# Performance work log

Measured on AMD Instinct MI355X. Metric: run time of the kernel, lower is better.

Reference implementation:

```python
import jax, jax.numpy as jnp
import numpy as np

N = 100000   # nodes
E = 1600000  # edges
G = 100      # graphs
M = 32       # m_dim for all layers


def _lin(k, din, dout):
    return (jax.random.normal(k, (din, dout), jnp.float32) / np.sqrt(din)).astype(jnp.float32)


def setup_inputs() -> dict:
    key = jax.random.key(0)
    ks = jax.random.split(key, 32)
    inp = {}
    inp["x"] = jax.random.normal(ks[0], (N, 2), jnp.float32)
    inp["positions"] = jax.random.normal(ks[1], (N, 2), jnp.float32)
    inp["edge_index"] = jax.random.randint(ks[2], (2, E), 0, N)
    inp["edge_attr"] = jax.random.normal(ks[3], (E, 1), jnp.float32)
    inp["batch"] = jnp.sort(jax.random.randint(ks[4], (N,), 0, G))
    ki = 5
    dims = [(2, 32), (32, 32), (32, 32)]  # (feats_in, out_dim) per EGNN layer
    for l, (fi, fo) in enumerate(dims, 1):
        ein = 2 * fi + 1 + 1  # x_i, x_j, edge_attr(1), rel_dist(1)
        inp[f"e{l}W1"] = _lin(ks[ki], ein, 2 * ein); ki += 1
        inp[f"e{l}b1"] = jnp.zeros((2 * ein,), jnp.float32)
        inp[f"e{l}W2"] = _lin(ks[ki], 2 * ein, M); ki += 1
        inp[f"e{l}b2"] = jnp.zeros((M,), jnp.float32)
        inp[f"n{l}W1"] = _lin(ks[ki], fi + M, 2 * fo); ki += 1
        inp[f"n{l}b1"] = jnp.zeros((2 * fo,), jnp.float32)
        inp[f"n{l}W2"] = _lin(ks[ki], 2 * fo, fo); ki += 1
        inp[f"n{l}b2"] = jnp.zeros((fo,), jnp.float32)
    inp["linW"] = _lin(ks[ki], 32, 1)
    inp["linb"] = jnp.zeros((1,), jnp.float32)
    return inp


def _egnn_layer(xcat, ei, ea, eW1, eb1, eW2, eb2, nW1, nb1, nW2, nb2):
    # xcat: [N, 2 + f_in]; coors pass through (update_coors=False)
    coors, feats = xcat[:, :2], xcat[:, 2:]
    j, i = ei[0], ei[1]  # PyG convention: edge_index[0]=source j, [1]=target i
    rel = coors[j] - coors[i]                      # [E, 2]
    rel_dist = jnp.sum(rel * rel, -1, keepdims=True)  # [E, 1]
    e_in = jnp.concatenate([feats[i], feats[j], ea, rel_dist], -1)
    m_ij = jax.nn.silu(jax.nn.silu(e_in @ eW1 + eb1) @ eW2 + eb2)  # [E, M]
    m_i = jax.ops.segment_sum(m_ij, i, num_segments=xcat.shape[0])  # aggr='add'
    h = jax.nn.silu(jnp.concatenate([feats, m_i], -1) @ nW1 + nb1) @ nW2 + nb2
    return jnp.concatenate([coors, h], -1)


def reference(x, edge_index, edge_attr, positions, batch,
              e1W1, e1b1, e1W2, e1b2, n1W1, n1b1, n1W2, n1b2,
              e2W1, e2b1, e2W2, e2b2, n2W1, n2b1, n2W2, n2b2,
              e3W1, e3b1, e3W2, e3b2, n3W1, n3b1, n3W2, n3b2,
              linW, linb):
    xt = jnp.concatenate([positions, x], -1).astype(jnp.float32)
    xt = _egnn_layer(xt, edge_index, edge_attr, e1W1, e1b1, e1W2, e1b2, n1W1, n1b1, n1W2, n1b2)
    xt = _egnn_layer(xt, edge_index, edge_attr, e2W1, e2b1, e2W2, e2b2, n2W1, n2b1, n2W2, n2b2)
    xt = _egnn_layer(xt, edge_index, edge_attr, e3W1, e3b1, e3W2, e3b2, n3W1, n3b1, n3W2, n3b2)
    feats = xt[:, 2:]  # drop coordinates
    cnt = jax.ops.segment_sum(jnp.ones((feats.shape[0],), jnp.float32), batch, num_segments=G)
    pooled = jax.ops.segment_sum(feats, batch, num_segments=G) / jnp.clip(cnt, 1.0)[:, None]
    return pooled @ linW + linb  # [G, 1]
```

## Files before the change

kernel.cpp:

```cpp
#include <hip/hip_runtime.h>
#include <hip/hip_bf16.h>

#define NN 100000
#define EE 1600000
#define GG 100

typedef __fp16 h2 __attribute__((ext_vector_type(2)));

#if __has_builtin(__builtin_amdgcn_fdot2)
#define FDOT2(a, b, c) __builtin_amdgcn_fdot2((a), (b), (c), false)
#else
__device__ __forceinline__ float FDOT2(h2 a, h2 b, float c) {
    return (float)a.x * (float)b.x + (float)a.y * (float)b.y + c;
}
#endif

__device__ __forceinline__ float silu_f(float x) {
    return x / (1.f + __expf(-x));
}

__device__ __forceinline__ float2 h2f2(unsigned int w) {
    h2 h = __builtin_bit_cast(h2, w);
    return make_float2((float)h.x, (float)h.y);
}


__global__ void k_hist(const int* __restrict__ ei, int* __restrict__ cnt) {
    int e = blockIdx.x * 256 + threadIdx.x;
    if (e >= EE) return;
    atomicAdd(&cnt[ei[EE + e]], 1);
}

__global__ void __launch_bounds__(1024) k_scan(const int* __restrict__ cnt,
                                               int* __restrict__ rowptr,
                                               int* __restrict__ head) {
    __shared__ int sdata[1024];
    int t = threadIdx.x;
    const int chunk = (NN + 1023) / 1024;
    int lo = t * chunk; if (lo > NN) lo = NN;
    int hi = lo + chunk; if (hi > NN) hi = NN;
    int s = 0;
    for (int n = lo; n < hi; n++) s += cnt[n];
    sdata[t] = s;
    __syncthreads();
    for (int off = 1; off < 1024; off <<= 1) {
        int val = (t >= off) ? sdata[t - off] : 0;
        __syncthreads();
        sdata[t] += val;
        __syncthreads();
    }
    int run = sdata[t] - s;
    for (int n = lo; n < hi; n++) {
        rowptr[n] = run; head[n] = run; run += cnt[n];
    }
    if (t == 0) rowptr[NN] = EE;
}

__global__ void k_scatter(const int* __restrict__ ei, const float* __restrict__ ea,
                          const float* __restrict__ pos, int* __restrict__ head,
                          float4* __restrict__ recs) {
    int e = blockIdx.x * 256 + threadIdx.x;
    if (e >= EE) return;
    int j = ei[e];
    int i = ei[EE + e];
    float dx = pos[2 * j] - pos[2 * i];
    float dy = pos[2 * j + 1] - pos[2 * i + 1];
    int p = atomicAdd(&head[i], 1);
    float4 r;
    r.x = __int_as_float(j);
    r.y = __int_as_float(i);
    r.z = ea[e];
    r.w = dx * dx + dy * dy;
    recs[p] = r;
}

template<int DH>
__global__ void k_packw2(const float* __restrict__ W2, h2* __restrict__ dst) {
    int idx = blockIdx.x * 256 + threadIdx.x;
    if (idx >= (DH / 2) * 32) return;
    int p = idx >> 5;
    int m = idx & 31;
    dst[idx] = __builtin_amdgcn_cvt_pkrtz(W2[(2 * p) * 32 + m], W2[(2 * p + 1) * 32 + m]);
}

template<int FI, int DH>
__global__ void k_uv(const float* __restrict__ feats, const float* __restrict__ W1,
                     __fp16* __restrict__ u, __fp16* __restrict__ v) {
    int idx = blockIdx.x * 256 + threadIdx.x;
    if (idx >= NN * DH) return;
    int n = idx / DH;
    int c = idx - n * DH;
    const float* f = feats + (size_t)n * FI;
    float su = 0.f, sv = 0.f;
#pragma unroll
    for (int k = 0; k < FI; k++) {
        float fk = f[k];
        su += fk * W1[k * DH + c];
        sv += fk * W1[(FI + k) * DH + c];
    }
    u[(size_t)n * DH + c] = (__fp16)su;
    v[(size_t)n * DH + c] = (__fp16)sv;
}

template<int FI, int DH>
__global__ void __launch_bounds__(256)
k_edge_agg(const __fp16* __restrict__ u, const __fp16* __restrict__ v,
           const float4* __restrict__ recs,
           const float* __restrict__ eW1, const float* __restrict__ eb1,
           const h2* __restrict__ w2pk, const float* __restrict__ eb2,
           float* __restrict__ mi) {
    constexpr int NC4 = DH / 4;
    constexpr int NP  = DH / 2;
    constexpr int GK  = (NC4 >= 11) ? 11 : NC4;
    constexpr int NGR = NC4 / GK;

    __shared__ __align__(16) float sA[DH], sB[DH], sb1[DH];
    __shared__ float sb2[32];
    __shared__ __align__(16) h2 sw2[NP * 32];

    for (int k = threadIdx.x; k < DH; k += 256) {
        sA[k]  = eW1[(2 * FI) * DH + k];
        sB[k]  = eW1[(2 * FI + 1) * DH + k];
        sb1[k] = eb1[k];
    }
    for (int k = threadIdx.x; k < NP * 32; k += 256) sw2[k] = w2pk[k];
    if (threadIdx.x < 32) sb2[threadIdx.x] = eb2[threadIdx.x];
    __syncthreads();

    int t = blockIdx.x * 256 + threadIdx.x;
    float4 r = recs[t];
    int j = __float_as_int(r.x);
    int i = __float_as_int(r.y);
    float eav = r.z;
    float rdv = r.w;
    const uint2* up = (const uint2*)(u + (size_t)i * DH);
    const uint2* vp = (const uint2*)(v + (size_t)j * DH);

    h2 hreg[NP];
#pragma unroll
    for (int g = 0; g < NGR; g++) {
        uint2 ub[GK], vb[GK];
#pragma unroll
        for (int k = 0; k < GK; k++) {
            ub[k] = up[g * GK + k];
            vb[k] = vp[g * GK + k];
        }
#pragma unroll
        for (int k = 0; k < GK; k++) {
            int c4 = g * GK + k;
            float2 u01 = h2f2(ub[k].x), u23 = h2f2(ub[k].y);
            float2 v01 = h2f2(vb[k].x), v23 = h2f2(vb[k].y);
            float4 a  = *(const float4*)&sA[c4 * 4];
            float4 b  = *(const float4*)&sB[c4 * 4];
            float4 bb = *(const float4*)&sb1[c4 * 4];
            float t0 = silu_f(u01.x + v01.x + eav * a.x + rdv * b.x + bb.x);
            float t1 = silu_f(u01.y + v01.y + eav * a.y + rdv * b.y + bb.y);
            float t2 = silu_f(u23.x + v23.x + eav * a.z + rdv * b.z + bb.z);
            float t3 = silu_f(u23.y + v23.y + eav * a.w + rdv * b.w + bb.w);
            hreg[2 * c4]     = __builtin_amdgcn_cvt_pkrtz(t0, t1);
            hreg[2 * c4 + 1] = __builtin_amdgcn_cvt_pkrtz(t2, t3);
        }
    }

    float acc[32];
#pragma unroll
    for (int m = 0; m < 32; m++) acc[m] = sb2[m];
#pragma unroll
    for (int mg = 0; mg < 8; mg++) {
#pragma unroll
        for (int p = 0; p < NP; p++) {
            uint4 W = *(const uint4*)(sw2 + p * 32 + mg * 4);
            acc[4 * mg + 0] = FDOT2(hreg[p], __builtin_bit_cast(h2, W.x), acc[4 * mg + 0]);
            acc[4 * mg + 1] = FDOT2(hreg[p], __builtin_bit_cast(h2, W.y), acc[4 * mg + 1]);
            acc[4 * mg + 2] = FDOT2(hreg[p], __builtin_bit_cast(h2, W.z), acc[4 * mg + 2]);
            acc[4 * mg + 3] = FDOT2(hreg[p], __builtin_bit_cast(h2, W.w), acc[4 * mg + 3]);
        }
    }
#pragma unroll
    for (int m = 0; m < 32; m++) acc[m] = silu_f(acc[m]);

    int lane = threadIdx.x & 63;
#pragma unroll
    for (int d = 1; d < 64; d <<= 1) {
        int oi = __shfl_down(i, d);
        bool take = (lane + d < 64) && (oi == i);
#pragma unroll
        for (int m = 0; m < 32; m++) {
            float ov = __shfl_down(acc[m], d);
            if (take) acc[m] += ov;
        }
    }
    int previ = __shfl_up(i, 1);
    int ilast = __shfl(i, 63);
    bool leader = (lane == 0) || (previ != i);
    if (leader) {
        float* row = mi + (size_t)i * 32;
        bool interior = (lane != 0) && (ilast != i);
        if (interior) {
            float4* row4 = (float4*)row;
#pragma unroll
            for (int q = 0; q < 8; q++)
                row4[q] = make_float4(acc[4 * q], acc[4 * q + 1], acc[4 * q + 2], acc[4 * q + 3]);
        } else {
#pragma unroll
            for (int m = 0; m < 32; m++) atomicAdd(row + m, acc[m]);
        }
    }
}

template<int FI, int NDH>
__global__ void __launch_bounds__(256)
k_node(const float* __restrict__ feats, const float* __restrict__ mi,
       const float* __restrict__ nW1, const float* __restrict__ nb1,
       const float* __restrict__ nW2, const float* __restrict__ nb2,
       float* __restrict__ fout,
       const float* __restrict__ eW1n,
       __fp16* __restrict__ un, __fp16* __restrict__ vn) {
    __shared__ float g_lds[4][64];
    __shared__ float s_f[4][32];
    int ln = threadIdx.x >> 6;
    int c  = threadIdx.x & 63;
    int n  = blockIdx.x * 4 + ln;
    float s = nb1[c];
    const float* f = feats + (size_t)n * FI;
#pragma unroll
    for (int k = 0; k < FI; k++) s += f[k] * nW1[k * 64 + c];
    const float* mrow = mi + (size_t)n * 32;
#pragma unroll
    for (int k = 0; k < 32; k++) s += mrow[k] * nW1[(FI + k) * 64 + c];
    g_lds[ln][c] = silu_f(s);
    __syncthreads();
    if (c < 32) {
        float o = nb2[c];
        const float* gr = g_lds[ln];
#pragma unroll
        for (int k = 0; k < 64; k++) o += gr[k] * nW2[k * 32 + c];
        fout[(size_t)n * 32 + c] = o;
        s_f[ln][c] = o;
    }
    if (NDH > 0) {
        __syncthreads();
        const float* fr = s_f[ln];
        for (int col = c; col < NDH; col += 64) {
            float su = 0.f, sv = 0.f;
#pragma unroll
            for (int k = 0; k < 32; k++) {
                float fk = fr[k];
                su += fk * eW1n[k * NDH + col];
                sv += fk * eW1n[(32 + k) * NDH + col];
            }
            un[(size_t)n * NDH + col] = (__fp16)su;
            vn[(size_t)n * NDH + col] = (__fp16)sv;
        }
    }
}

__global__ void k_pool(const float* __restrict__ feats, const int* __restrict__ batch,
                       const float* __restrict__ linW, const float* __restrict__ linb,
                       float* __restrict__ out) {
    int g = blockIdx.x;
    __shared__ int s_lo, s_hi;
    if (threadIdx.x == 0) {
        int lo = 0, hi = NN;
        while (lo < hi) { int mid = (lo + hi) >> 1; if (batch[mid] < g) lo = mid + 1; else hi = mid; }
        s_lo = lo;
    }
    if (threadIdx.x == 1) {
        int lo = 0, hi = NN;
        while (lo < hi) { int mid = (lo + hi) >> 1; if (batch[mid] < g + 1) lo = mid + 1; else hi = mid; }
        s_hi = lo;
    }
    __syncthreads();
    int lo = s_lo, hi = s_hi;
    int m = threadIdx.x & 31;
    int r = threadIdx.x >> 5;
    float s = 0.f;
    for (int n = lo + r; n < hi; n += 8) s += feats[(size_t)n * 32 + m];
    __shared__ float sm[8][32];
    sm[r][m] = s;
    __syncthreads();
    if (threadIdx.x == 0) {
        float cntf = (float)((hi - lo) > 0 ? (hi - lo) : 1);
        float tot = 0.f;
        for (int mm = 0; mm < 32; mm++) {
            float colsum = 0.f;
            for (int rr = 0; rr < 8; rr++) colsum += sm[rr][mm];
            tot += (colsum / cntf) * linW[mm];
        }
        out[g] = tot + linb[0];
    }
}

extern "C" void kernel_launch(void* const* d_in, const int* in_sizes, int n_in,
                              void* d_out, int out_size, void* d_ws, size_t ws_size,
                              hipStream_t stream) {
    const float* x    = (const float*)d_in[0];
    const float* pos  = (const float*)d_in[1];
    const int*   ei   = (const int*)d_in[2];
    const float* ea   = (const float*)d_in[3];
    const int*   bat  = (const int*)d_in[4];
    const float* W[24];
    for (int k = 0; k < 24; k++) W[k] = (const float*)d_in[5 + k];
    const float* linW = (const float*)d_in[29];
    const float* linb = (const float*)d_in[30];
    float* out = (float*)d_out;

    char* p = (char*)d_ws;
    float4*  recs = (float4*)p;         p += (size_t)EE * 16;
    __fp16*  u    = (__fp16*)p;         p += (size_t)NN * 132 * 2;
    __fp16*  v    = (__fp16*)p;         p += (size_t)NN * 132 * 2;
    float*   mi   = (float*)p;          p += (size_t)NN * 32 * 4;
    float*   f    = (float*)p;          p += (size_t)NN * 32 * 4;
    h2*      w2p1 = (h2*)p;             p += (size_t)(6  * 32) * 4;
    h2*      w2p2 = (h2*)p;             p += (size_t)(66 * 32) * 4;
    h2*      w2p3 = (h2*)p;             p += (size_t)(66 * 32) * 4;
    int*     cnt  = (int*)p;            p += (size_t)NN * 4;
    int*     rowptr = (int*)p;          p += (size_t)(NN + 4) * 4;
    int*     head = (int*)p;            p += (size_t)NN * 4;

    (void)hipMemsetAsync(cnt, 0, (size_t)NN * 4, stream);
    k_hist<<<EE / 256, 256, 0, stream>>>(ei, cnt);
    k_scan<<<1, 1024, 0, stream>>>(cnt, rowptr, head);
    k_scatter<<<EE / 256, 256, 0, stream>>>(ei, ea, pos, head, recs);
    k_packw2<12> <<<1, 256, 0, stream>>>(W[2],  w2p1);
    k_packw2<132><<<(66 * 32 + 255) / 256, 256, 0, stream>>>(W[10], w2p2);
    k_packw2<132><<<(66 * 32 + 255) / 256, 256, 0, stream>>>(W[18], w2p3);

    k_uv<2, 12><<<(NN * 12 + 255) / 256, 256, 0, stream>>>(x, W[0], u, v);
    (void)hipMemsetAsync(mi, 0, (size_t)NN * 32 * 4, stream);
    k_edge_agg<2, 12><<<EE / 256, 256, 0, stream>>>(u, v, recs, W[0], W[1], w2p1, W[3], mi);
    k_node<2, 132><<<NN / 4, 256, 0, stream>>>(x, mi, W[4], W[5], W[6], W[7], f, W[8], u, v);

    (void)hipMemsetAsync(mi, 0, (size_t)NN * 32 * 4, stream);
    k_edge_agg<32, 132><<<EE / 256, 256, 0, stream>>>(u, v, recs, W[8], W[9], w2p2, W[11], mi);
    k_node<32, 132><<<NN / 4, 256, 0, stream>>>(f, mi, W[12], W[13], W[14], W[15], f, W[16], u, v);

    (void)hipMemsetAsync(mi, 0, (size_t)NN * 32 * 4, stream);
    k_edge_agg<32, 132><<<EE / 256, 256, 0, stream>>>(u, v, recs, W[16], W[17], w2p3, W[19], mi);
    k_node<32, 0><<<NN / 4, 256, 0, stream>>>(f, mi, W[20], W[21], W[22], W[23], f, nullptr, nullptr, nullptr);

    k_pool<<<GG, 256, 0, stream>>>(f, bat, linW, linb, out);
}
```

Baseline: 1.912 ms.

## Use MFMA for second edge-MLP layer in layers 2 and 3

Replaces the per-thread FDOT2 loop for the 132x32 second edge linear with 16x16x16 f16 MFMA instructions. Each wave stages its hidden activations in LDS, and the weights are pre-packed into B fragments. The segmented reduction moves from 32-register shuffles to an LDS transpose plus a serial per-column run-length scan with atomics at run boundaries. The change adds about 76KB of LDS per block, which lowers occupancy, and the serial 32-step scan may limit the gain.

```diff
diff --git a/kernel.cpp b/kernel.cpp
--- a/kernel.cpp
+++ b/kernel.cpp
@@ -6,6 +6,8 @@
 #define GG 100
 
 typedef __fp16 h2 __attribute__((ext_vector_type(2)));
+typedef __fp16 h4v __attribute__((ext_vector_type(4)));
+typedef float f4v __attribute__((ext_vector_type(4)));
 
 #if __has_builtin(__builtin_amdgcn_fdot2)
 #define FDOT2(a, b, c) __builtin_amdgcn_fdot2((a), (b), (c), false)
@@ -13,6 +15,18 @@
 __device__ __forceinline__ float FDOT2(h2 a, h2 b, float c) {
     return (float)a.x * (float)b.x + (float)a.y * (float)b.y + c;
 }
+#endif
+
+#if __has_builtin(__builtin_amdgcn_mfma_f32_16x16x16f16)
+#define MFMA16(a, b, c) __builtin_amdgcn_mfma_f32_16x16x16f16((a), (b), (c), 0, 0, 0)
+#elif __has_builtin(__builtin_amdgcn_mfma_f32_16x16x16_f16)
+#define MFMA16(a, b, c) __builtin_amdgcn_mfma_f32_16x16x16_f16((a), (b), (c), 0, 0, 0)
+#else
+__device__ __forceinline__ f4v mfma16_asm(h4v a, h4v b, f4v c) {
+    asm volatile("v_mfma_f32_16x16x16_f16 %0, %1, %2, %0" : "+v"(c) : "v"(a), "v"(b));
+    return c;
+}
+#define MFMA16(a, b, c) mfma16_asm((a), (b), (c))
 #endif
 
 __device__ __forceinline__ float silu_f(float x) {
@@ -83,6 +97,24 @@
     dst[idx] = __builtin_amdgcn_cvt_pkrtz(W2[(2 * p) * 32 + m], W2[(2 * p + 1) * 32 + m]);
 }
 
+__global__ void k_packBfrag(const float* __restrict__ W2, __fp16* __restrict__ dst) {
+    int idx = blockIdx.x * 256 + threadIdx.x;
+    if (idx >= 9 * 2 * 64) return;
+    int l   = idx & 63;
+    int snt = idx >> 6;
+    int s   = snt >> 1;
+    int nt  = snt & 1;
+    int n   = (nt << 4) + (l & 15);
+    int kb  = s * 16 + ((l >> 4) << 2);
+    h4v val;
+#pragma unroll
+    for (int q = 0; q < 4; q++) {
+        int k = kb + q;
+        val[q] = (k < 132) ? (__fp16)W2[k * 32 + n] : (__fp16)0.f;
+    }
+    *(h4v*)(dst + (size_t)idx * 4) = val;
+}
+
 template<int FI, int DH>
 __global__ void k_uv(const float* __restrict__ feats, const float* __restrict__ W1,
                      __fp16* __restrict__ u, __fp16* __restrict__ v) {
@@ -111,8 +143,6 @@
            float* __restrict__ mi) {
     constexpr int NC4 = DH / 4;
     constexpr int NP  = DH / 2;
-    constexpr int GK  = (NC4 >= 11) ? 11 : NC4;
-    constexpr int NGR = NC4 / GK;
 
     __shared__ __align__(16) float sA[DH], sB[DH], sb1[DH];
     __shared__ float sb2[32];
@@ -137,6 +167,109 @@
     const uint2* vp = (const uint2*)(v + (size_t)j * DH);
 
     h2 hreg[NP];
+#pragma unroll
+    for (int c4 = 0; c4 < NC4; c4++) {
+        uint2 uu = up[c4];
+        uint2 vv = vp[c4];
+        float2 u01 = h2f2(uu.x), u23 = h2f2(uu.y);
+        float2 v01 = h2f2(vv.x), v23 = h2f2(vv.y);
+        float4 a  = *(const float4*)&sA[c4 * 4];
+        float4 b  = *(const float4*)&sB[c4 * 4];
+        float4 bb = *(const float4*)&sb1[c4 * 4];
+        float t0 = silu_f(u01.x + v01.x + eav * a.x + rdv * b.x + bb.x);
+        float t1 = silu_f(u01.y + v01.y + eav * a.y + rdv * b.y + bb.y);
+        float t2 = silu_f(u23.x + v23.x + eav * a.z + rdv * b.z + bb.z);
+        float t3 = silu_f(u23.y + v23.y + eav * a.w + rdv * b.w + bb.w);
+        hreg[2 * c4]     = __builtin_amdgcn_cvt_pkrtz(t0, t1);
+        hreg[2 * c4 + 1] = __builtin_amdgcn_cvt_pkrtz(t2, t3);
+    }
+
+    float acc[32];
+#pragma unroll
+    for (int m = 0; m < 32; m++) acc[m] = sb2[m];
+#pragma unroll
+    for (int mg = 0; mg < 8; mg++) {
+#pragma unroll
+        for (int p = 0; p < NP; p++) {
+            uint4 W = *(const uint4*)(sw2 + p * 32 + mg * 4);
+            acc[4 * mg + 0] = FDOT2(hreg[p], __builtin_bit_cast(h2, W.x), acc[4 * mg + 0]);
+            acc[4 * mg + 1] = FDOT2(hreg[p], __builtin_bit_cast(h2, W.y), acc[4 * mg + 1]);
+            acc[4 * mg + 2] = FDOT2(hreg[p], __builtin_bit_cast(h2, W.z), acc[4 * mg + 2]);
+            acc[4 * mg + 3] = FDOT2(hreg[p], __builtin_bit_cast(h2, W.w), acc[4 * mg + 3]);
+        }
+    }
+#pragma unroll
+    for (int m = 0; m < 32; m++) acc[m] = silu_f(acc[m]);
+
+    int lane = threadIdx.x & 63;
+#pragma unroll
+    for (int d = 1; d < 64; d <<= 1) {
+        int oi = __shfl_down(i, d);
+        bool take = (lane + d < 64) && (oi == i);
+#pragma unroll
+        for (int m = 0; m < 32; m++) {
+            float ov = __shfl_down(acc[m], d);
+            if (take) acc[m] += ov;
+        }
+    }
+    int previ = __shfl_up(i, 1);
+    int ilast = __shfl(i, 63);
+    bool leader = (lane == 0) || (previ != i);
+    if (leader) {
+        float* row = mi + (size_t)i * 32;
+        bool interior = (lane != 0) && (ilast != i);
+        if (interior) {
+            float4* row4 = (float4*)row;
+#pragma unroll
+            for (int q = 0; q < 8; q++)
+                row4[q] = make_float4(acc[4 * q], acc[4 * q + 1], acc[4 * q + 2], acc[4 * q + 3]);
+        } else {
+#pragma unroll
+            for (int m = 0; m < 32; m++) atomicAdd(row + m, acc[m]);
+        }
+    }
+}
+
+#define H1_STRIDE 148
+#define WAVE_LDS_BYTES (64 * H1_STRIDE * 2)
+#define W_OFF 1728
+
+__global__ void __launch_bounds__(256)
+k_edge_mfma(const __fp16* __restrict__ u, const __fp16* __restrict__ v,
+            const float4* __restrict__ recs,
+            const float* __restrict__ eW1, const float* __restrict__ eb1,
+            const __fp16* __restrict__ w2f, const float* __restrict__ eb2,
+            float* __restrict__ mi) {
+    constexpr int FI = 32, DH = 132, NC4 = 33, GK = 11, NGR = 3;
+
+    __shared__ __align__(16) char smem[W_OFF + 4 * WAVE_LDS_BYTES];
+    float* sA  = (float*)smem;
+    float* sB  = sA + 132;
+    float* sb1 = sB + 132;
+    float* sb2 = sb1 + 132;
+
+    for (int k = threadIdx.x; k < DH; k += 256) {
+        sA[k]  = eW1[(2 * FI) * DH + k];
+        sB[k]  = eW1[(2 * FI + 1) * DH + k];
+        sb1[k] = eb1[k];
+    }
+    if (threadIdx.x < 32) sb2[threadIdx.x] = eb2[threadIdx.x];
+    __syncthreads();
+
+    int wid  = threadIdx.x >> 6;
+    int lane = threadIdx.x & 63;
+    __fp16* h1w = (__fp16*)(smem + W_OFF + wid * WAVE_LDS_BYTES);
+
+    int t = blockIdx.x * 256 + threadIdx.x;
+    float4 r = recs[t];
+    int j = __float_as_int(r.x);
+    int i = __float_as_int(r.y);
+    float eav = r.z;
+    float rdv = r.w;
+    const uint2* up = (const uint2*)(u + (size_t)i * DH);
+    const uint2* vp = (const uint2*)(v + (size_t)j * DH);
+
+    h2 hreg[66];
 #pragma unroll
     for (int g = 0; g < NGR; g++) {
         uint2 ub[GK], vb[GK];
@@ -162,50 +295,77 @@
         }
     }
 
-    float acc[32];
-#pragma unroll
-    for (int m = 0; m < 32; m++) acc[m] = sb2[m];
-#pragma unroll
-    for (int mg = 0; mg < 8; mg++) {
-#pragma unroll
-        for (int p = 0; p < NP; p++) {
-            uint4 W = *(const uint4*)(sw2 + p * 32 + mg * 4);
-            acc[4 * mg + 0] = FDOT2(hreg[p], __builtin_bit_cast(h2, W.x), acc[4 * mg + 0]);
-            acc[4 * mg + 1] = FDOT2(hreg[p], __builtin_bit_cast(h2, W.y), acc[4 * mg + 1]);
-            acc[4 * mg + 2] = FDOT2(hreg[p], __builtin_bit_cast(h2, W.z), acc[4 * mg + 2]);
-            acc[4 * mg + 3] = FDOT2(hreg[p], __builtin_bit_cast(h2, W.w), acc[4 * mg + 3]);
-        }
-    }
-#pragma unroll
-    for (int m = 0; m < 32; m++) acc[m] = silu_f(acc[m]);
-
-    int lane = threadIdx.x & 63;
-#pragma unroll
-    for (int d = 1; d < 64; d <<= 1) {
-        int oi = __shfl_down(i, d);
-        bool take = (lane + d < 64) && (oi == i);
-#pragma unroll
-        for (int m = 0; m < 32; m++) {
-            float ov = __shfl_down(acc[m], d);
-            if (take) acc[m] += ov;
-        }
-    }
-    int previ = __shfl_up(i, 1);
-    int ilast = __shfl(i, 63);
-    bool leader = (lane == 0) || (previ != i);
-    if (leader) {
-        float* row = mi + (size_t)i * 32;
-        bool interior = (lane != 0) && (ilast != i);
-        if (interior) {
-            float4* row4 = (float4*)row;
-#pragma unroll
-            for (int q = 0; q < 8; q++)
-                row4[q] = make_float4(acc[4 * q], acc[4 * q + 1], acc[4 * q + 2], acc[4 * q + 3]);
+    __fp16* hrow = h1w + lane * H1_STRIDE;
+#pragma unroll
+    for (int p = 0; p < 33; p++) {
+        uint2 w;
+        w.x = __builtin_bit_cast(unsigned int, hreg[2 * p]);
+        w.y = __builtin_bit_cast(unsigned int, hreg[2 * p + 1]);
+        *(uint2*)(hrow + 4 * p) = w;
+    }
+    *(uint2*)(hrow + 132) = make_uint2(0u, 0u);
+    *(uint2*)(hrow + 136) = make_uint2(0u, 0u);
+    *(uint2*)(hrow + 140) = make_uint2(0u, 0u);
+
+    h4v bf[9][2];
+#pragma unroll
+    for (int s = 0; s < 9; s++) {
+#pragma unroll
+        for (int nt = 0; nt < 2; nt++)
+            bf[s][nt] = *(const h4v*)(w2f + ((size_t)((s * 2 + nt) * 64 + lane)) * 4);
+    }
+
+    int c15 = lane & 15;
+    int g4  = (lane >> 4) << 2;
+    float b2lo = sb2[c15], b2hi = sb2[16 + c15];
+    f4v acc[4][2];
+#pragma unroll
+    for (int mt = 0; mt < 4; mt++) {
+        acc[mt][0] = (f4v){b2lo, b2lo, b2lo, b2lo};
+        acc[mt][1] = (f4v){b2hi, b2hi, b2hi, b2hi};
+    }
+#pragma unroll
+    for (int s = 0; s < 9; s++) {
+#pragma unroll
+        for (int mt = 0; mt < 4; mt++) {
+            h4v a = *(const h4v*)(h1w + (16 * mt + c15) * H1_STRIDE + s * 16 + g4);
+            acc[mt][0] = MFMA16(a, bf[s][0], acc[mt][0]);
+            acc[mt][1] = MFMA16(a, bf[s][1], acc[mt][1]);
+        }
+    }
+
+    float* Db = (float*)h1w;
+    int*   ib = (int*)(Db + 64 * 33);
+    ib[lane] = i;
+#pragma unroll
+    for (int mt = 0; mt < 4; mt++) {
+#pragma unroll
+        for (int q = 0; q < 4; q++) {
+            int e = 16 * mt + g4 + q;
+            Db[e * 33 + c15]      = silu_f(acc[mt][0][q]);
+            Db[e * 33 + 16 + c15] = silu_f(acc[mt][1][q]);
+        }
+    }
+    __syncthreads();
+
+    int half = lane >> 5, c = lane & 31;
+    int e0 = half << 5, e1 = e0 + 32;
+    float racc = Db[e0 * 33 + c];
+    int icur = ib[e0];
+    int rstart = e0;
+    for (int e = e0 + 1; e < e1; e++) {
+        int ie = ib[e];
+        float val = Db[e * 33 + c];
+        if (ie != icur) {
+            float* dst = mi + (size_t)icur * 32 + c;
+            if (rstart > e0) *dst = racc;
+            else atomicAdd(dst, racc);
+            racc = val; icur = ie; rstart = e;
         } else {
-#pragma unroll
-            for (int m = 0; m < 32; m++) atomicAdd(row + m, acc[m]);
-        }
-    }
+            racc += val;
+        }
+    }
+    atomicAdd(mi + (size_t)icur * 32 + c, racc);
 }
 
 template<int FI, int NDH>
@@ -311,9 +471,9 @@
     __fp16*  v    = (__fp16*)p;         p += (size_t)NN * 132 * 2;
     float*   mi   = (float*)p;          p += (size_t)NN * 32 * 4;
     float*   f    = (float*)p;          p += (size_t)NN * 32 * 4;
-    h2*      w2p1 = (h2*)p;             p += (size_t)(6  * 32) * 4;
-    h2*      w2p2 = (h2*)p;             p += (size_t)(66 * 32) * 4;
-    h2*      w2p3 = (h2*)p;             p += (size_t)(66 * 32) * 4;
+    h2*      w2p1 = (h2*)p;             p += (size_t)(6 * 32) * 4;
+    __fp16*  w2f2 = (__fp16*)p;         p += (size_t)(9 * 2 * 64 * 4) * 2;
+    __fp16*  w2f3 = (__fp16*)p;         p += (size_t)(9 * 2 * 64 * 4) * 2;
     int*     cnt  = (int*)p;            p += (size_t)NN * 4;
     int*     rowptr = (int*)p;          p += (size_t)(NN + 4) * 4;
     int*     head = (int*)p;            p += (size_t)NN * 4;
@@ -322,9 +482,9 @@
     k_hist<<<EE / 256, 256, 0, stream>>>(ei, cnt);
     k_scan<<<1, 1024, 0, stream>>>(cnt, rowptr, head);
     k_scatter<<<EE / 256, 256, 0, stream>>>(ei, ea, pos, head, recs);
-    k_packw2<12> <<<1, 256, 0, stream>>>(W[2],  w2p1);
-    k_packw2<132><<<(66 * 32 + 255) / 256, 256, 0, stream>>>(W[10], w2p2);
-    k_packw2<132><<<(66 * 32 + 255) / 256, 256, 0, stream>>>(W[18], w2p3);
+    k_packw2<12><<<1, 256, 0, stream>>>(W[2], w2p1);
+    k_packBfrag<<<5, 256, 0, stream>>>(W[10], w2f2);
+    k_packBfrag<<<5, 256, 0, stream>>>(W[18], w2f3);
 
     k_uv<2, 12><<<(NN * 12 + 255) / 256, 256, 0, stream>>>(x, W[0], u, v);
     (void)hipMemsetAsync(mi, 0, (size_t)NN * 32 * 4, stream);
@@ -332,11 +492,11 @@
     k_node<2, 132><<<NN / 4, 256, 0, stream>>>(x, mi, W[4], W[5], W[6], W[7], f, W[8], u, v);
 
     (void)hipMemsetAsync(mi, 0, (size_t)NN * 32 * 4, stream);
-    k_edge_agg<32, 132><<<EE / 256, 256, 0, stream>>>(u, v, recs, W[8], W[9], w2p2, W[11], mi);
+    k_edge_mfma<<<EE / 256, 256, 0, stream>>>(u, v, recs, W[8], W[9], w2f2, W[11], mi);
     k_node<32, 132><<<NN / 4, 256, 0, stream>>>(f, mi, W[12], W[13], W[14], W[15], f, W[16], u, v);
 
     (void)hipMemsetAsync(mi, 0, (size_t)NN * 32 * 4, stream);
-    k_edge_agg<32, 132><<<EE / 256, 256, 0, stream>>>(u, v, recs, W[16], W[17], w2p3, W[19], mi);
+    k_edge_mfma<<<EE / 256, 256, 0, stream>>>(u, v, recs, W[16], W[17], w2f3, W[19], mi);
     k_node<32, 0><<<NN / 4, 256, 0, stream>>>(f, mi, W[20], W[21], W[22], W[23], f, nullptr, nullptr, nullptr);
 
     k_pool<<<GG, 256, 0, stream>>>(f, bat, linW, linb, out);
```

Measured after the change: 1.717 ms. -10.2%, faster.
